# Kernel tuning notes

Measured on AMD Instinct MI355X. Metric: run time of the kernel, lower is better.

Reference implementation:

```python
import jax, jax.numpy as jnp
import numpy as np

G = 4          # number of product sub-quantizers
K = 1024       # codebook_size per sub-quantizer
D = 256        # full feature dim
d = D // G     # sub-dim per quantizer
DECAY = 0.99
EPS = 1e-5


def setup_inputs() -> dict:
    key = jax.random.key(0)
    k1, k2, k3, k4 = jax.random.split(key, 4)
    x = jax.random.normal(k1, (8, 4096, D), jnp.float32)
    embed = jax.random.normal(k2, (G, K, d), jnp.float32)
    embed_avg = jax.random.normal(k3, (G, K, d), jnp.float32)
    cluster_size = jax.random.uniform(k4, (G, K), jnp.float32)
    return dict(x=x, embed=embed, embed_avg=embed_avg, cluster_size=cluster_size)


def reference(x, embed, embed_avg, cluster_size):
    B, S, _ = x.shape
    N = B * S
    xg = x.reshape(N, G, d)                       # [N, G, d] tokens split into sub-vectors
    x2 = jnp.sum(xg * xg, axis=-1, keepdims=True)  # [N, G, 1]
    e2 = jnp.sum(embed * embed, axis=-1)           # [G, K]
    dots = jnp.einsum('ngd,gkd->ngk', xg, embed)   # [N, G, K]
    dist = -(x2 - 2.0 * dots + e2[None, :, :])     # [N, G, K]
    # sample_codebook_temp = 0 -> gumbel_sample degenerates to argmax
    ind = jnp.argmax(dist, axis=-1)                # [N, G]
    # quantized vectors: gather from each group's codebook
    zq = embed[jnp.arange(G)[None, :], ind]        # [N, G, d]
    # --- EMA buffer updates (training path) via scatter/segment-sum ---
    flat_ids = (ind + jnp.arange(G)[None, :] * K).reshape(-1)  # [N*G]
    counts = jax.ops.segment_sum(
        jnp.ones_like(flat_ids, dtype=jnp.float32), flat_ids,
        num_segments=G * K).reshape(G, K)
    embed_sum = jax.ops.segment_sum(
        xg.reshape(N * G, d), flat_ids,
        num_segments=G * K).reshape(G, K, d)
    new_cluster_size = DECAY * cluster_size + (1.0 - DECAY) * counts
    new_embed_avg = DECAY * embed_avg + (1.0 - DECAY) * embed_sum
    # laplace smoothing then renormalize codebook
    tot = jnp.sum(new_cluster_size, axis=-1, keepdims=True)       # [G, 1]
    smoothed = (new_cluster_size + EPS) / (tot + K * EPS) * tot   # [G, K]
    new_embed = new_embed_avg / smoothed[..., None]               # [G, K, d]
    return (zq.reshape(B, S, D),
            ind.reshape(B, S, G).astype(jnp.int32),
            new_embed, new_cluster_size, new_embed_avg)
```

## Files before the change

kernel.cpp:

```cpp
#include <hip/hip_runtime.h>
#include <cstdint>

#define GQ 4
#define KQ 1024
#define DQ 256
#define dq 64
#define NQ 32768
#define DECAYF 0.99f
#define EPSF 1e-5f

#define OFF_ZQ    0
#define OFF_IND   8388608
#define OFF_EMB   8519680
#define OFF_CS    8781824
#define OFF_AVG   8785920

#define WS_IND   0
#define WS_E2    524288
#define WS_EH    540672
#define WS_EL    1064960
#define WS_CTR   1589264
#define WS_LIST  1589280
#define CAP      16384
#define WS_E2D   1720352
#define WS_TOT   1753120
#define WS_PART  1753344
#define WS_PCNT  10141952

#define MARGIN 0.01f
#define FPS 65536.0f

#define MBLK 64

typedef __attribute__((ext_vector_type(8))) short bf16x8;
typedef __attribute__((ext_vector_type(4))) float f32x4;

__device__ __forceinline__ void split8_2x(float4 u, float4 v, bf16x8& h, bf16x8& l) {
    float f[8] = {u.x, u.y, u.z, u.w, v.x, v.y, v.z, v.w};
#pragma unroll
    for (int j = 0; j < 8; ++j) {
        float s = f[j] * 2.0f;
        uint32_t b = __float_as_uint(s);
        uint32_t hb = b & 0xffff0000u;
        float r = s - __uint_as_float(hb);
        uint32_t rb = __float_as_uint(r);
        h[j] = (short)(hb >> 16);
        l[j] = (short)((rb + 0x7fffu + ((rb >> 16) & 1u)) >> 16);
    }
}

__global__ void k_prep(const float* __restrict__ embed, const float* __restrict__ cs,
                       float* __restrict__ e2, double* __restrict__ e2d,
                       ushort* __restrict__ eh, ushort* __restrict__ el,
                       float* __restrict__ tot, int* __restrict__ ctr) {
    __shared__ double red[256];
    int t = blockIdx.x * 256 + threadIdx.x;
    int row = t >> 3;
    int f = t & 7;
    int c = f >> 2, l4 = f & 3;
    int g = row >> 10, k = row & 1023;
    int ch = k >> 6, co = k & 63;

    const float4* p = reinterpret_cast<const float4*>(embed + (size_t)row * dq + f * 8);
    float4 u = p[0], v = p[1];
    float fv[8] = {u.x, u.y, u.z, u.w, v.x, v.y, v.z, v.w};
    bf16x8 h, l;
    double s = 0.0;
#pragma unroll
    for (int jj = 0; jj < 8; ++jj) {
        float x = fv[jj];
        s = fma((double)x, (double)x, s);
        uint32_t b = __float_as_uint(x);
        uint32_t hb = (b + 0x7fffu + ((b >> 16) & 1u)) & 0xffff0000u;
        float r = x - __uint_as_float(hb);
        uint32_t rb = __float_as_uint(r);
        h[jj] = (short)(hb >> 16);
        l[jj] = (short)((rb + 0x7fffu + ((rb >> 16) & 1u)) >> 16);
    }
    size_t addr = (size_t)g * 65536 + (size_t)ch * 4096 + (size_t)(c * 4 + l4) * 512 + co * 8;
    *reinterpret_cast<bf16x8*>(eh + addr) = h;
    *reinterpret_cast<bf16x8*>(el + addr) = l;
    s += __shfl_xor(s, 1, 64);
    s += __shfl_xor(s, 2, 64);
    s += __shfl_xor(s, 4, 64);
    if (f == 0) { e2[row] = (float)s; e2d[row] = s; }

    if (blockIdx.x < 4) {
        int gg = blockIdx.x;
        const float4* c4 = reinterpret_cast<const float4*>(cs + gg * KQ);
        float4 cv = c4[threadIdx.x];
        red[threadIdx.x] = (double)cv.x + (double)cv.y + (double)cv.z + (double)cv.w;
        __syncthreads();
        for (int off = 128; off > 0; off >>= 1) {
            if (threadIdx.x < off) red[threadIdx.x] += red[threadIdx.x + off];
            __syncthreads();
        }
        if (threadIdx.x == 0) {
            tot[gg] = (float)((double)DECAYF * red[0] + (1.0 - (double)DECAYF) * (double)NQ);
            if (gg == 0) *ctr = 0;
        }
    }
}

__launch_bounds__(256)
__global__ void k_scores_mfma(const float* __restrict__ x,
                              const ushort* __restrict__ eh,
                              const ushort* __restrict__ el,
                              const float* __restrict__ e2,
                              const float* __restrict__ embed,
                              int* __restrict__ ind_t,
                              float* __restrict__ zq,
                              float* __restrict__ ind_out,
                              int* __restrict__ ctr, int2* __restrict__ list) {
    int g = blockIdx.y;
    int n0 = blockIdx.x * MBLK;
    int tid = threadIdx.x;
    int wid = tid >> 6;
    int lane = tid & 63;
    int l15 = lane & 15, l4 = lane >> 4;

    __shared__ ushort lds[2][8192];

    bf16x8 ah[2], al[2];
#pragma unroll
    for (int c = 0; c < 2; ++c) {
        const float4* p = reinterpret_cast<const float4*>(
            x + (size_t)(n0 + wid * 16 + l15) * DQ + g * dq + c * 32 + l4 * 8);
        split8_2x(p[0], p[1], ah[c], al[c]);
    }

    const ushort* ehg = eh + (size_t)g * 65536;
    const ushort* elg = el + (size_t)g * 65536;
    const float*  e2g = e2 + (size_t)g * KQ;

    float m1[4], m2[4];
    int   k1[4];
#pragma unroll
    for (int r = 0; r < 4; ++r) { m1[r] = -3.4e38f; m2[r] = -3.4e38f; k1[r] = 0; }

    int wu = wid * 512;
#define STAGE(b, ch)                                                               \
    do {                                                                           \
        const ushort* s0_ = ehg + (ch) * 4096 + tid * 8;                           \
        const ushort* s1_ = elg + (ch) * 4096 + tid * 8;                           \
        __builtin_amdgcn_global_load_lds(s0_,        &lds[b][wu],        16, 0, 0);\
        __builtin_amdgcn_global_load_lds(s0_ + 2048, &lds[b][2048 + wu], 16, 0, 0);\
        __builtin_amdgcn_global_load_lds(s1_,        &lds[b][4096 + wu], 16, 0, 0);\
        __builtin_amdgcn_global_load_lds(s1_ + 2048, &lds[b][6144 + wu], 16, 0, 0);\
    } while (0)

    float e2cur[4];
#pragma unroll
    for (int n = 0; n < 4; ++n) e2cur[n] = e2g[n * 16 + l15];

    STAGE(0, 0);
    int cur = 0;

#pragma unroll 1
    for (int ch = 0; ch < 16; ++ch) {
        int cb = ch * 64;
        __syncthreads();
        if (ch < 15) STAGE(cur ^ 1, ch + 1);

        float e2nxt[4];
        if (ch < 15) {
#pragma unroll
            for (int n = 0; n < 4; ++n) e2nxt[n] = e2g[cb + 64 + n * 16 + l15];
        }

        f32x4 acc[4];
#pragma unroll
        for (int n = 0; n < 4; ++n)
            acc[n] = (f32x4){-e2cur[n], -e2cur[n], -e2cur[n], -e2cur[n]};

#pragma unroll
        for (int c = 0; c < 2; ++c) {
            bf16x8 bh[4], bl[4];
            int base = (c * 4 + l4) * 512 + l15 * 8;
#pragma unroll
            for (int n = 0; n < 4; ++n) {
                bh[n] = *reinterpret_cast<const bf16x8*>(&lds[cur][base + n * 128]);
                bl[n] = *reinterpret_cast<const bf16x8*>(&lds[cur][4096 + base + n * 128]);
            }
#pragma unroll
            for (int n = 0; n < 4; ++n) {
                acc[n] = __builtin_amdgcn_mfma_f32_16x16x32_bf16(ah[c], bh[n], acc[n], 0, 0, 0);
                acc[n] = __builtin_amdgcn_mfma_f32_16x16x32_bf16(ah[c], bl[n], acc[n], 0, 0, 0);
                acc[n] = __builtin_amdgcn_mfma_f32_16x16x32_bf16(al[c], bh[n], acc[n], 0, 0, 0);
            }
        }

#pragma unroll
        for (int n = 0; n < 4; ++n) {
            int col = cb + n * 16 + l15;
#pragma unroll
            for (int r = 0; r < 4; ++r) {
                float s = acc[n][r];
                bool gt = s > m1[r];
                m2[r] = __builtin_amdgcn_fmed3f(s, m1[r], m2[r]);
                k1[r] = gt ? col : k1[r];
                m1[r] = fmaxf(m1[r], s);
            }
        }
#pragma unroll
        for (int n = 0; n < 4; ++n) e2cur[n] = e2nxt[n];
        cur ^= 1;
    }
#undef STAGE

    int* ckk = reinterpret_cast<int*>(&lds[0][0]);

#pragma unroll
    for (int r = 0; r < 4; ++r) {
        float a1 = m1[r], a2 = m2[r];
        int ak = k1[r];
#pragma unroll
        for (int d = 1; d < 16; d <<= 1) {
            float o1 = __shfl_xor(a1, d, 64);
            float o2 = __shfl_xor(a2, d, 64);
            int   ok = __shfl_xor(ak, d, 64);
            bool sw = (o1 > a1) || (o1 == a1 && ok < ak);
            float big = sw ? o1 : a1;
            int bigk = sw ? ok : ak;
            float small = sw ? a1 : o1;
            a2 = fmaxf(fmaxf(a2, o2), small);
            a1 = big; ak = bigk;
        }
        if (l15 == 0) {
            int rloc = l4 * 4 + r;
            int row = n0 + wid * 16 + rloc;
            ckk[wid * 16 + rloc] = ak;
            ind_t[(size_t)g * NQ + row] = ak;
            if (a1 - a2 < MARGIN) {
                int idx = atomicAdd(ctr, 1);
                if (idx < CAP) list[idx] = make_int2(row, g);
            }
        }
    }
    __syncthreads();

    if (lane < 16) {
        int row = n0 + wid * 16 + lane;
        ind_out[(size_t)row * GQ + g] = (float)ckk[wid * 16 + lane];
    }
#pragma unroll 4
    for (int rr = 0; rr < 16; ++rr) {
        int k = ckk[wid * 16 + rr];
        float v = embed[((size_t)(g * KQ + k)) * dq + lane];
        zq[(size_t)(n0 + wid * 16 + rr) * DQ + g * dq + lane] = v;
    }
}

__launch_bounds__(256)
__global__ void k_recheck(const float* __restrict__ x, const float* __restrict__ embed,
                          const double* __restrict__ e2d,
                          const int* __restrict__ ctr, const int2* __restrict__ list,
                          int* __restrict__ ind_t, float* __restrict__ zq,
                          float* __restrict__ ind_out) {
    __shared__ double sv[256];
    __shared__ int si[256];
    int nitems = *ctr;
    if (nitems > CAP) nitems = CAP;
    for (int it = blockIdx.x; it < nitems; it += gridDim.x) {
        int2 q = list[it];
        int n = q.x, g = q.y;
        const float4* xr4 = reinterpret_cast<const float4*>(x + (size_t)n * DQ + g * dq);
        float4 xr[16];
#pragma unroll
        for (int j = 0; j < 16; ++j) xr[j] = xr4[j];
        double best = -1e300;
        int bk = KQ;
        for (int k = threadIdx.x; k < KQ; k += 256) {
            const float4* er = reinterpret_cast<const float4*>(embed + ((size_t)g * KQ + k) * dq);
            double dot = 0.0;
#pragma unroll
            for (int j = 0; j < 16; ++j) {
                float4 e4 = er[j];
                dot = fma((double)xr[j].x, (double)e4.x, dot);
                dot = fma((double)xr[j].y, (double)e4.y, dot);
                dot = fma((double)xr[j].z, (double)e4.z, dot);
                dot = fma((double)xr[j].w, (double)e4.w, dot);
            }
            double s = 2.0 * dot - e2d[g * KQ + k];
            if (s > best || (s == best && k < bk)) { best = s; bk = k; }
        }
        sv[threadIdx.x] = best; si[threadIdx.x] = bk;
        __syncthreads();
        for (int off = 128; off > 0; off >>= 1) {
            if (threadIdx.x < off) {
                double ov = sv[threadIdx.x + off]; int oi = si[threadIdx.x + off];
                if (ov > sv[threadIdx.x] || (ov == sv[threadIdx.x] && oi < si[threadIdx.x])) {
                    sv[threadIdx.x] = ov; si[threadIdx.x] = oi;
                }
            }
            __syncthreads();
        }
        int kbest = si[0];
        if (threadIdx.x == 0) {
            ind_t[(size_t)g * NQ + n] = kbest;
            ind_out[(size_t)n * GQ + g] = (float)kbest;
        }
        if (threadIdx.x < dq)
            zq[(size_t)n * DQ + g * dq + threadIdx.x] =
                embed[((size_t)g * KQ + kbest) * dq + threadIdx.x];
        __syncthreads();
    }
}

#define SBINS 32
__launch_bounds__(256)
__global__ void k_segsum4(const float* __restrict__ x, const int* __restrict__ ind_t,
                          int* __restrict__ partial, int* __restrict__ pcnt) {
    __shared__ int lacc[SBINS][64];
    __shared__ int lcnt[SBINS];
    __shared__ int queue[4][128];

    int bid = blockIdx.x;
    int g = bid >> 8;
    int grp = (bid >> 3) & 31;
    int split = bid & 7;
    int kbase = grp * SBINS;
    int tid = threadIdx.x, wid = tid >> 6, lane = tid & 63;

    for (int i = tid; i < SBINS * 64; i += 256) ((int*)lacc)[i] = 0;
    if (tid < SBINS) lcnt[tid] = 0;
    __syncthreads();

    const int* ip = ind_t + (size_t)g * NQ;
    const float* xg = x + g * dq;
    int nbase = split * 4096 + wid * 1024;
    int wqn = 0;

#define DRAIN4                                                                      \
    do {                                                                            \
        int nq4 = wqn & ~3;                                                         \
        for (int q = 0; q < nq4; q += 4) {                                          \
            int ea = queue[wid][q],     eb = queue[wid][q + 1];                     \
            int ec = queue[wid][q + 2], ed = queue[wid][q + 3];                     \
            float va = xg[(size_t)(ea & 0xfffff) * DQ + lane];                      \
            float vb = xg[(size_t)(eb & 0xfffff) * DQ + lane];                      \
            float vc = xg[(size_t)(ec & 0xfffff) * DQ + lane];                      \
            float vd = xg[(size_t)(ed & 0xfffff) * DQ + lane];                      \
            atomicAdd(&lacc[ea >> 20][lane], __float2int_rn(va * FPS));             \
            atomicAdd(&lacc[eb >> 20][lane], __float2int_rn(vb * FPS));             \
            atomicAdd(&lacc[ec >> 20][lane], __float2int_rn(vc * FPS));             \
            atomicAdd(&lacc[ed >> 20][lane], __float2int_rn(vd * FPS));             \
            if (lane == 0) {                                                        \
                atomicAdd(&lcnt[ea >> 20], 1); atomicAdd(&lcnt[eb >> 20], 1);       \
                atomicAdd(&lcnt[ec >> 20], 1); atomicAdd(&lcnt[ed >> 20], 1);       \
            }                                                                       \
        }                                                                           \
        for (int q = nq4; q < wqn; ++q) {                                           \
            int e = queue[wid][q];                                                  \
            float v = xg[(size_t)(e & 0xfffff) * DQ + lane];                        \
            atomicAdd(&lacc[e >> 20][lane], __float2int_rn(v * FPS));               \
            if (lane == 0) atomicAdd(&lcnt[e >> 20], 1);                            \
        }                                                                           \
        wqn = 0;                                                                    \
    } while (0)

    for (int c = 0; c < 1024; c += 64) {
        int n = nbase + c + lane;
        int d = ip[n] - kbase;
        bool hit = (unsigned)d < (unsigned)SBINS;
        unsigned long long mask = __ballot(hit);
        if (hit) {
            int pos = wqn + __popcll(mask & ((1ull << lane) - 1ull));
            queue[wid][pos] = (d << 20) | n;
        }
        wqn += __popcll(mask);
        if (wqn >= 64) DRAIN4;
    }
    DRAIN4;
#undef DRAIN4
    __syncthreads();

    int base = split * (GQ * KQ) + g * KQ + kbase;
    for (int i = tid; i < SBINS * 64; i += 256) {
        int b = i >> 6, l = i & 63;
        partial[(size_t)(base + b) * 64 + l] = lacc[b][l];
    }
    if (tid < SBINS) pcnt[base + tid] = lcnt[tid];
}

__global__ void k_final(const int* __restrict__ partial, const int* __restrict__ pcnt,
                        const float* __restrict__ embed_avg, const float* __restrict__ cs,
                        const float* __restrict__ tot,
                        float* __restrict__ out_cs, float* __restrict__ out_avg,
                        float* __restrict__ out_embed) {
    int t = blockIdx.x * 256 + threadIdx.x;
    int gk = t >> 6, l = t & 63, g = gk >> 10;
    const int GK = GQ * KQ;
    int s = 0, c = 0;
#pragma unroll
    for (int sp = 0; sp < 8; ++sp) {
        s += partial[((size_t)sp * GK + gk) * 64 + l];
        c += pcnt[sp * GK + gk];
    }
    float a = (float)s * (1.0f / FPS);
    float nea = DECAYF * embed_avg[t] + (1.0f - DECAYF) * a;
    out_avg[t] = nea;
    float ncs = DECAYF * cs[gk] + (1.0f - DECAYF) * (float)c;
    if (l == 0) out_cs[gk] = ncs;
    double tt = (double)tot[g];
    double sm = ((double)ncs + (double)EPSF) / (tt + (double)KQ * (double)EPSF) * tt;
    out_embed[t] = nea / (float)sm;
}

extern "C" void kernel_launch(void* const* d_in, const int* in_sizes, int n_in,
                              void* d_out, int out_size, void* d_ws, size_t ws_size,
                              hipStream_t stream) {
    const float* x         = (const float*)d_in[0];
    const float* embed     = (const float*)d_in[1];
    const float* embed_avg = (const float*)d_in[2];
    const float* cs        = (const float*)d_in[3];
    float* out = (float*)d_out;
    float* zq        = out + OFF_ZQ;
    float* ind_out   = out + OFF_IND;
    float* out_embed = out + OFF_EMB;
    float* out_cs    = out + OFF_CS;
    float* out_avg   = out + OFF_AVG;

    char* ws = (char*)d_ws;
    int*    ind_t = (int*)(ws + WS_IND);
    float*  e2    = (float*)(ws + WS_E2);
    ushort* eh    = (ushort*)(ws + WS_EH);
    ushort* el    = (ushort*)(ws + WS_EL);
    int*    ctr   = (int*)(ws + WS_CTR);
    int2*   list  = (int2*)(ws + WS_LIST);
    double* e2d   = (double*)(ws + WS_E2D);
    float*  tot   = (float*)(ws + WS_TOT);
    int*    part  = (int*)(ws + WS_PART);
    int*    pcnt  = (int*)(ws + WS_PCNT);

    k_prep<<<128, 256, 0, stream>>>(embed, cs, e2, e2d, eh, el, tot, ctr);
    dim3 g1(NQ / MBLK, GQ);
    k_scores_mfma<<<g1, 256, 0, stream>>>(x, eh, el, e2, embed, ind_t, zq, ind_out, ctr, list);
    k_recheck<<<256, 256, 0, stream>>>(x, embed, e2d, ctr, list, ind_t, zq, ind_out);
    k_segsum4<<<1024, 256, 0, stream>>>(x, ind_t, part, pcnt);
    k_final<<<(GQ * KQ * dq) / 256, 256, 0, stream>>>(part, pcnt, embed_avg, cs, tot,
                                                      out_cs, out_avg, out_embed);
}
```

Before: 129.5 us.

## Switch score kernel to 32x32x16 MFMA with 128-row blocks

```diff
diff --git a/kernel.cpp b/kernel.cpp
--- a/kernel.cpp
+++ b/kernel.cpp
@@ -30,10 +30,11 @@
 #define MARGIN 0.01f
 #define FPS 65536.0f
 
-#define MBLK 64
+#define MBLK 128
 
 typedef __attribute__((ext_vector_type(8))) short bf16x8;
 typedef __attribute__((ext_vector_type(4))) float f32x4;
+typedef __attribute__((ext_vector_type(16))) float f32x16;
 
 __device__ __forceinline__ void split8_2x(float4 u, float4 v, bf16x8& h, bf16x8& l) {
     float f[8] = {u.x, u.y, u.z, u.w, v.x, v.y, v.z, v.w};
@@ -57,7 +58,6 @@
     int t = blockIdx.x * 256 + threadIdx.x;
     int row = t >> 3;
     int f = t & 7;
-    int c = f >> 2, l4 = f & 3;
     int g = row >> 10, k = row & 1023;
     int ch = k >> 6, co = k & 63;
 
@@ -77,7 +77,8 @@
         h[jj] = (short)(hb >> 16);
         l[jj] = (short)((rb + 0x7fffu + ((rb >> 16) & 1u)) >> 16);
     }
-    size_t addr = (size_t)g * 65536 + (size_t)ch * 4096 + (size_t)(c * 4 + l4) * 512 + co * 8;
+    size_t addr = (size_t)g * 65536 + (size_t)ch * 4096 + (size_t)(f >> 1) * 1024
+                + (size_t)(co >> 5) * 512 + (size_t)((f & 1) * 32 + (co & 31)) * 8;
     *reinterpret_cast<bf16x8*>(eh + addr) = h;
     *reinterpret_cast<bf16x8*>(el + addr) = l;
     s += __shfl_xor(s, 1, 64);
@@ -117,26 +118,26 @@
     int tid = threadIdx.x;
     int wid = tid >> 6;
     int lane = tid & 63;
-    int l15 = lane & 15, l4 = lane >> 4;
+    int l31 = lane & 31, lhi = lane >> 5;
 
     __shared__ ushort lds[2][8192];
 
-    bf16x8 ah[2], al[2];
-#pragma unroll
-    for (int c = 0; c < 2; ++c) {
+    bf16x8 ah[4], al[4];
+#pragma unroll
+    for (int kb = 0; kb < 4; ++kb) {
         const float4* p = reinterpret_cast<const float4*>(
-            x + (size_t)(n0 + wid * 16 + l15) * DQ + g * dq + c * 32 + l4 * 8);
-        split8_2x(p[0], p[1], ah[c], al[c]);
+            x + (size_t)(n0 + wid * 32 + l31) * DQ + g * dq + kb * 16 + lhi * 8);
+        split8_2x(p[0], p[1], ah[kb], al[kb]);
     }
 
     const ushort* ehg = eh + (size_t)g * 65536;
     const ushort* elg = el + (size_t)g * 65536;
     const float*  e2g = e2 + (size_t)g * KQ;
 
-    float m1[4], m2[4];
-    int   k1[4];
-#pragma unroll
-    for (int r = 0; r < 4; ++r) { m1[r] = -3.4e38f; m2[r] = -3.4e38f; k1[r] = 0; }
+    float m1[16], m2[16];
+    int   k1[16];
+#pragma unroll
+    for (int r = 0; r < 16; ++r) { m1[r] = -3.4e38f; m2[r] = -3.4e38f; k1[r] = 0; }
 
     int wu = wid * 512;
 #define STAGE(b, ch)                                                               \
@@ -149,9 +150,9 @@
         __builtin_amdgcn_global_load_lds(s1_ + 2048, &lds[b][6144 + wu], 16, 0, 0);\
     } while (0)
 
-    float e2cur[4];
-#pragma unroll
-    for (int n = 0; n < 4; ++n) e2cur[n] = e2g[n * 16 + l15];
+    float e2cur[2];
+    e2cur[0] = e2g[l31];
+    e2cur[1] = e2g[32 + l31];
 
     STAGE(0, 0);
     int cur = 0;
@@ -162,39 +163,39 @@
         __syncthreads();
         if (ch < 15) STAGE(cur ^ 1, ch + 1);
 
-        float e2nxt[4];
+        float e2nxt[2];
         if (ch < 15) {
-#pragma unroll
-            for (int n = 0; n < 4; ++n) e2nxt[n] = e2g[cb + 64 + n * 16 + l15];
-        }
-
-        f32x4 acc[4];
-#pragma unroll
-        for (int n = 0; n < 4; ++n)
-            acc[n] = (f32x4){-e2cur[n], -e2cur[n], -e2cur[n], -e2cur[n]};
-
-#pragma unroll
-        for (int c = 0; c < 2; ++c) {
-            bf16x8 bh[4], bl[4];
-            int base = (c * 4 + l4) * 512 + l15 * 8;
-#pragma unroll
-            for (int n = 0; n < 4; ++n) {
-                bh[n] = *reinterpret_cast<const bf16x8*>(&lds[cur][base + n * 128]);
-                bl[n] = *reinterpret_cast<const bf16x8*>(&lds[cur][4096 + base + n * 128]);
+            e2nxt[0] = e2g[cb + 64 + l31];
+            e2nxt[1] = e2g[cb + 96 + l31];
+        }
+
+        f32x16 acc[2];
+#pragma unroll
+        for (int n = 0; n < 2; ++n)
+#pragma unroll
+            for (int r = 0; r < 16; ++r) acc[n][r] = -e2cur[n];
+
+#pragma unroll
+        for (int kb = 0; kb < 4; ++kb) {
+            bf16x8 bh[2], bl[2];
+            int base = kb * 1024 + lane * 8;
+            bh[0] = *reinterpret_cast<const bf16x8*>(&lds[cur][base]);
+            bh[1] = *reinterpret_cast<const bf16x8*>(&lds[cur][base + 512]);
+            bl[0] = *reinterpret_cast<const bf16x8*>(&lds[cur][4096 + base]);
+            bl[1] = *reinterpret_cast<const bf16x8*>(&lds[cur][4096 + base + 512]);
+#pragma unroll
+            for (int n = 0; n < 2; ++n) {
+                acc[n] = __builtin_amdgcn_mfma_f32_32x32x16_bf16(ah[kb], bh[n], acc[n], 0, 0, 0);
+                acc[n] = __builtin_amdgcn_mfma_f32_32x32x16_bf16(ah[kb], bl[n], acc[n], 0, 0, 0);
+                acc[n] = __builtin_amdgcn_mfma_f32_32x32x16_bf16(al[kb], bh[n], acc[n], 0, 0, 0);
             }
-#pragma unroll
-            for (int n = 0; n < 4; ++n) {
-                acc[n] = __builtin_amdgcn_mfma_f32_16x16x32_bf16(ah[c], bh[n], acc[n], 0, 0, 0);
-                acc[n] = __builtin_amdgcn_mfma_f32_16x16x32_bf16(ah[c], bl[n], acc[n], 0, 0, 0);
-                acc[n] = __builtin_amdgcn_mfma_f32_16x16x32_bf16(al[c], bh[n], acc[n], 0, 0, 0);
-            }
-        }
-
-#pragma unroll
-        for (int n = 0; n < 4; ++n) {
-            int col = cb + n * 16 + l15;
-#pragma unroll
-            for (int r = 0; r < 4; ++r) {
+        }
+
+#pragma unroll
+        for (int n = 0; n < 2; ++n) {
+            int col = cb + n * 32 + l31;
+#pragma unroll
+            for (int r = 0; r < 16; ++r) {
                 float s = acc[n][r];
                 bool gt = s > m1[r];
                 m2[r] = __builtin_amdgcn_fmed3f(s, m1[r], m2[r]);
@@ -202,8 +203,8 @@
                 m1[r] = fmaxf(m1[r], s);
             }
         }
-#pragma unroll
-        for (int n = 0; n < 4; ++n) e2cur[n] = e2nxt[n];
+        e2cur[0] = e2nxt[0];
+        e2cur[1] = e2nxt[1];
         cur ^= 1;
     }
 #undef STAGE
@@ -211,11 +212,11 @@
     int* ckk = reinterpret_cast<int*>(&lds[0][0]);
 
 #pragma unroll
-    for (int r = 0; r < 4; ++r) {
+    for (int r = 0; r < 16; ++r) {
         float a1 = m1[r], a2 = m2[r];
         int ak = k1[r];
 #pragma unroll
-        for (int d = 1; d < 16; d <<= 1) {
+        for (int d = 1; d < 32; d <<= 1) {
             float o1 = __shfl_xor(a1, d, 64);
             float o2 = __shfl_xor(a2, d, 64);
             int   ok = __shfl_xor(ak, d, 64);
@@ -226,10 +227,10 @@
             a2 = fmaxf(fmaxf(a2, o2), small);
             a1 = big; ak = bigk;
         }
-        if (l15 == 0) {
-            int rloc = l4 * 4 + r;
-            int row = n0 + wid * 16 + rloc;
-            ckk[wid * 16 + rloc] = ak;
+        if (l31 == 0) {
+            int rloc = (r & 3) + 8 * (r >> 2) + 4 * lhi;
+            int row = n0 + wid * 32 + rloc;
+            ckk[wid * 32 + rloc] = ak;
             ind_t[(size_t)g * NQ + row] = ak;
             if (a1 - a2 < MARGIN) {
                 int idx = atomicAdd(ctr, 1);
@@ -239,15 +240,15 @@
     }
     __syncthreads();
 
-    if (lane < 16) {
-        int row = n0 + wid * 16 + lane;
-        ind_out[(size_t)row * GQ + g] = (float)ckk[wid * 16 + lane];
+    if (lane < 32) {
+        int row = n0 + wid * 32 + lane;
+        ind_out[(size_t)row * GQ + g] = (float)ckk[wid * 32 + lane];
     }
 #pragma unroll 4
-    for (int rr = 0; rr < 16; ++rr) {
-        int k = ckk[wid * 16 + rr];
+    for (int rr = 0; rr < 32; ++rr) {
+        int k = ckk[wid * 32 + rr];
         float v = embed[((size_t)(g * KQ + k)) * dq + lane];
-        zq[(size_t)(n0 + wid * 16 + rr) * DQ + g * dq + lane] = v;
+        zq[(size_t)(n0 + wid * 32 + rr) * DQ + g * dq + lane] = v;
     }
 }
 
```

Result: slower. 135.2 us (+4.4%).
